# Optimization experiments

Hardware: AMD Instinct MI355X
Metric: run time of the kernel (lower is better)

Reference implementation:

```python
import jax, jax.numpy as jnp
import numpy as np

MAXDISP = 48
NUM_GROUPS = 40
CONCAT_CH = 12
BN_EPS = 1e-5


def conv3d(x, w):
    # x: [B,C,D,H,W], w: [O,I,3,3,3], stride 1, pad 1
    return jax.lax.conv_general_dilated(
        x, w, window_strides=(1, 1, 1), padding=[(1, 1), (1, 1), (1, 1)],
        dimension_numbers=('NCDHW', 'OIDHW', 'NCDHW'))


def bn_relu(x, gamma, beta, mean, var):
    # inference-style BatchNorm3d followed by ReLU
    inv = gamma * jax.lax.rsqrt(var + BN_EPS)
    sh = (1, -1, 1, 1, 1)
    return jax.nn.relu(x * inv.reshape(sh) + (beta - mean * inv).reshape(sh))


def build_volume(lg, rg, lc, rc):
    # Fused gwc + concat volume: for disparity d, valid region is columns [d:].
    # Columns [:d] are zero (matches the torch new_zeros + sliced writes).
    B, Cg, H, W = lg.shape
    cpg = Cg // NUM_GROUPS
    slices = []
    for d in range(MAXDISP):  # fixed structural loop over disparities
        if d == 0:
            l, r, lcc, rcc = lg, rg, lc, rc
        else:
            l = lg[:, :, :, d:]
            r = rg[:, :, :, :W - d]
            lcc = lc[:, :, :, d:]
            rcc = rc[:, :, :, :W - d]
        corr = (l * r).reshape(B, NUM_GROUPS, cpg, H, W - d).mean(axis=2)
        s = jnp.concatenate([corr, lcc, rcc], axis=1)  # [B, G+2Cc, H, W-d]
        if d > 0:
            s = jnp.pad(s, ((0, 0), (0, 0), (0, 0), (d, 0)))
        slices.append(s)
    return jnp.stack(slices, axis=2)  # [B, G+2Cc, D, H, W]


def setup_inputs() -> dict:
    key = jax.random.key(0)
    ks = jax.random.split(key, 10)
    B, H, W = 4, 64, 128
    Cin = NUM_GROUPS + 2 * CONCAT_CH  # 64
    f32 = jnp.float32
    return {
        'left_gwc': jax.random.normal(ks[0], (B, 320, H, W), f32),
        'right_gwc': jax.random.normal(ks[1], (B, 320, H, W), f32),
        'left_concat': jax.random.normal(ks[2], (B, CONCAT_CH, H, W), f32),
        'right_concat': jax.random.normal(ks[3], (B, CONCAT_CH, H, W), f32),
        'w1': jax.random.normal(ks[4], (32, Cin, 3, 3, 3), f32) * 0.05,
        'g1': jnp.ones((32,), f32),
        'b1': jnp.zeros((32,), f32),
        'm1': jnp.zeros((32,), f32),
        'v1': jnp.ones((32,), f32),
        'w2': jax.random.normal(ks[5], (32, 32, 3, 3, 3), f32) * 0.05,
        'g2': jnp.ones((32,), f32),
        'b2': jnp.zeros((32,), f32),
        'm2': jnp.zeros((32,), f32),
        'v2': jnp.ones((32,), f32),
    }


def reference(left_gwc, right_gwc, left_concat, right_concat,
              w1, g1, b1, m1, v1, w2, g2, b2, m2, v2):
    vol = build_volume(left_gwc, right_gwc, left_concat, right_concat)
    x = bn_relu(conv3d(vol, w1), g1, b1, m1, v1)
    x = bn_relu(conv3d(x, w2), g2, b2, m2, v2)
    return x  # [B, 32, D, H, W]
```

## Files before the change

### kernel.cpp

```cpp
#include <hip/hip_runtime.h>
#include <cstdint>
#include <cstddef>

typedef unsigned short u16;
typedef __bf16 bf16x8 __attribute__((ext_vector_type(8)));
typedef float f32x4 __attribute__((ext_vector_type(4)));

#define MAXDISP 48
#define HH 64
#define WW 128

__device__ __forceinline__ float bf2f(unsigned int x) {
    union { unsigned int i; float f; } c; c.i = x << 16; return c.f;
}
__device__ __forceinline__ float bf2f_hi(unsigned int x) {
    union { unsigned int i; float f; } c; c.i = x & 0xffff0000u; return c.f;
}
__device__ __forceinline__ u16 f2bf(float f) {
    union { float f; unsigned int i; } c; c.f = f;
    unsigned int x = c.i;
    return (u16)((x + 0x7fffu + ((x >> 16) & 1u)) >> 16);
}

__global__ __launch_bounds__(256) void wfrag_kernel(
    const float* __restrict__ w, const float* __restrict__ gam,
    const float* __restrict__ bet, const float* __restrict__ mea,
    const float* __restrict__ var,
    u16* __restrict__ dst, float* __restrict__ bias, int CIN, int KC)
{
    int idx = blockIdx.x * 256 + threadIdx.x;
    int n = 9 * 2 * KC * 512;
    if (idx < n) {
        int j    = idx & 7;
        int lane = (idx >> 3) & 63;
        int t2   = idx >> 9;
        int kc   = t2 % KC;
        int t3   = t2 / KC;
        int nt   = t3 & 1;
        int tap  = t3 >> 1;
        int co   = nt * 16 + (lane & 15);
        int qq   = lane >> 4;
        int kw, c;
        if (CIN == 64) { kw = kc >> 1; c = (kc & 1) * 32 + qq * 8 + j; }
        else           { kw = kc;      c = qq * 8 + j; }
        int kd = tap / 3, kh = tap % 3;
        float inv = gam[co] * rsqrtf(var[co] + 1e-5f);
        dst[idx] = f2bf(w[((size_t)co * CIN + c) * 27 + kd * 9 + kh * 3 + kw] * inv);
    }
    if (blockIdx.x == 0 && threadIdx.x < 32) {
        int co = threadIdx.x;
        float inv = gam[co] * rsqrtf(var[co] + 1e-5f);
        bias[co] = bet[co] - mea[co] * inv;
    }
}

#define RS 334
__global__ __launch_bounds__(512) void vol_build_kernel(
    const float* __restrict__ lg, const float* __restrict__ rg,
    const float* __restrict__ lc, const float* __restrict__ rc,
    u16* __restrict__ vol)
{
    __shared__ u16 r_s[128 * RS];
    __shared__ u16 o_s[4 * 128 * 68];

    int bi  = blockIdx.x;
    int h   = bi & 63;
    int dh  = (bi >> 6) & 1;
    int b   = bi >> 7;
    u16* volr = vol + (size_t)(b >> 1) * 50331648;
    int bl  = b & 1;
    int tid = threadIdx.x;
    int w    = tid & 127;
    int part = tid >> 7;

    for (int idx = tid; idx < 320 * 32; idx += 512) {
        int c = idx >> 5, w4 = (idx & 31) << 2;
        const float4 v = *(const float4*)(rg + (((size_t)b * 320 + c) * 64 + h) * 128 + w4);
        r_s[(w4 + 0) * RS + c] = f2bf(v.x);
        r_s[(w4 + 1) * RS + c] = f2bf(v.y);
        r_s[(w4 + 2) * RS + c] = f2bf(v.z);
        r_s[(w4 + 3) * RS + c] = f2bf(v.w);
    }
    for (int idx = tid; idx < 12 * 32; idx += 512) {
        int c = idx >> 5, w4 = (idx & 31) << 2;
        const float4 v = *(const float4*)(rc + (((size_t)b * 12 + c) * 64 + h) * 128 + w4);
        r_s[(w4 + 0) * RS + 320 + c] = f2bf(v.x);
        r_s[(w4 + 1) * RS + 320 + c] = f2bf(v.y);
        r_s[(w4 + 2) * RS + 320 + c] = f2bf(v.z);
        r_s[(w4 + 3) * RS + 320 + c] = f2bf(v.w);
    }
    u16 lcv[12];
    if (part == 0) {
#pragma unroll
        for (int k = 0; k < 12; k++)
            lcv[k] = f2bf(lc[(((size_t)b * 12 + k) * 64 + h) * 128 + w]);
    }
    __syncthreads();

    int d0 = dh * 24;
    for (int dc = 0; dc < 24; dc += 4) {
        for (int gb = 0; gb < 5; gb++) {
            int g0 = part * 10 + gb * 2;
            float lv[2][8];
#pragma unroll
            for (int gg = 0; gg < 2; gg++)
#pragma unroll
                for (int j = 0; j < 8; j++)
                    lv[gg][j] = lg[(((size_t)b * 320 + (g0 + gg) * 8 + j) * 64 + h) * 128 + w];
#pragma unroll
            for (int dl = 0; dl < 4; dl++) {
                int d = d0 + dc + dl;
                union { u16 us[2]; unsigned int u1; } pk;
                pk.us[0] = pk.us[1] = 0;
                if (w >= d) {
#pragma unroll
                    for (int gg = 0; gg < 2; gg++) {
                        float s = 0.f;
                        int base = (w - d) * RS + (g0 + gg) * 8;
#pragma unroll
                        for (int jj = 0; jj < 4; jj++) {
                            unsigned int uu = *(const unsigned int*)&r_s[base + jj * 2];
                            s += lv[gg][jj * 2]     * bf2f(uu & 0xffffu);
                            s += lv[gg][jj * 2 + 1] * bf2f_hi(uu);
                        }
                        pk.us[gg] = f2bf(s * 0.125f);
                    }
                }
                *(unsigned int*)&o_s[(dl * 128 + w) * 68 + g0] = pk.u1;
            }
        }
#pragma unroll
        for (int dl = 0; dl < 4; dl++) {
            int d = d0 + dc + dl;
            union { u16 us[12]; uint2 u2[3]; } z;
            if (part == 0) {
#pragma unroll
                for (int k = 0; k < 12; k++) z.us[k] = (w >= d) ? lcv[k] : (u16)0;
                u16* dst = &o_s[(dl * 128 + w) * 68 + 40];
                *(uint2*)(dst + 0) = z.u2[0];
                *(uint2*)(dst + 4) = z.u2[1];
                *(uint2*)(dst + 8) = z.u2[2];
            } else if (part == 1) {
                if (w >= d) {
                    int base = (w - d) * RS + 320;
#pragma unroll
                    for (int k = 0; k < 12; k++) z.us[k] = r_s[base + k];
                } else {
#pragma unroll
                    for (int k = 0; k < 12; k++) z.us[k] = 0;
                }
                u16* dst = &o_s[(dl * 128 + w) * 68 + 52];
                *(uint2*)(dst + 0) = z.u2[0];
                *(uint2*)(dst + 4) = z.u2[1];
                *(uint2*)(dst + 8) = z.u2[2];
            }
        }
        __syncthreads();
#pragma unroll
        for (int i = 0; i < 8; i++) {
            int idx = i * 512 + tid;
            int dl  = idx >> 10;
            int rem = idx & 1023;
            int ww  = rem >> 3, cg = rem & 7;
            const u16* sp = &o_s[(dl * 128 + ww) * 68 + cg * 8];
            uint2 lo = *(const uint2*)sp;
            uint2 hi = *(const uint2*)(sp + 4);
            uint4 ov = { lo.x, lo.y, hi.x, hi.y };
            int d = d0 + dc + dl;
            *(uint4*)(volr + ((((size_t)bl * 48 + d) * 64 + h) * 128 + ww) * 64
                             + ((cg ^ ((ww + 1) & 7)) << 3)) = ov;
        }
        __syncthreads();
    }
}

__global__ __launch_bounds__(256) void conv1_mfma_kernel(
    const u16* __restrict__ vol, const u16* __restrict__ wf,
    const float* __restrict__ bias, u16* __restrict__ x1)
{
    __shared__ u16 a_s[2][130 * 64];

    int p  = blockIdx.x;
    int bi = (p & 7) * 768 + (p >> 3);
    int h  = bi & 63;
    int t1 = bi >> 6;
    int d  = t1 % 48;
    int bl = t1 / 48;
    int tid  = threadIdx.x;
    int lane = tid & 63, wid = tid >> 6;
    int lm = lane & 15, q = lane >> 4;

    if (tid < 32) {
        uint4 z = { 0, 0, 0, 0 };
        int bb = tid >> 4, t = tid & 15;
        int wp = (t >> 3) ? 129 : 0;
        *(uint4*)&a_s[bb][wp * 64 + (t & 7) * 8] = z;
    }

    f32x4 acc[2][2];
#pragma unroll
    for (int i = 0; i < 2; i++)
#pragma unroll
        for (int j = 0; j < 2; j++) acc[i][j] = { 0.f, 0.f, 0.f, 0.f };

    const size_t blb = (size_t)bl * 48;

    auto stage = [&](int bb, int kd_, int kh_) {
        int dd = d + kd_ - 1; dd = dd < 0 ? 0 : (dd > 47 ? 47 : dd);
        int hh = h + kh_ - 1; hh = hh < 0 ? 0 : (hh > 63 ? 63 : hh);
        const u16* src = vol + ((blb + (size_t)dd) * 64 + hh) * 8192;
        u16* dst = &a_s[bb][64];
#pragma unroll
        for (int i = 0; i < 4; i++) {
            __builtin_amdgcn_global_load_lds(
                (const __attribute__((address_space(1))) unsigned int*)(const void*)(src + (i * 256 + tid) * 8),
                (__attribute__((address_space(3))) unsigned int*)(void*)(dst + (i * 256 + tid) * 8),
                16, 0, 0);
        }
    };

    stage(0, 0, 0);
    __syncthreads();

#pragma unroll
    for (int kd = 0; kd < 3; kd++) {
#pragma unroll
        for (int kh = 0; kh < 3; kh++) {
            const int tap = kd * 3 + kh;
            bool valid = (kd == 0 ? (d > 0) : (kd == 2 ? (d < 47) : true))
                      && (kh == 0 ? (h > 0) : (kh == 2 ? (h < 63) : true));

            bf16x8 bfr[2][6];
            if (valid) {
#pragma unroll
                for (int nt = 0; nt < 2; nt++)
#pragma unroll
                    for (int kc = 0; kc < 6; kc++)
                        bfr[nt][kc] = *(const bf16x8*)(wf + (((size_t)tap * 2 + nt) * 6 + kc) * 512 + lane * 8);
            }
            __builtin_amdgcn_sched_barrier(0);
            if (tap < 8) stage((tap + 1) & 1, (tap + 1) / 3, (tap + 1) % 3);

            if (valid) {
                const u16* as = a_s[tap & 1];
#pragma unroll
                for (int kc = 0; kc < 6; kc++) {
                    int kw = kc >> 1;
                    int cg = (kc & 1) * 4 + q;
#pragma unroll
                    for (int mt = 0; mt < 2; mt++) {
                        int wp = (wid * 2 + mt) * 16 + lm + kw;
                        bf16x8 afr = *(const bf16x8*)&as[wp * 64 + ((cg ^ (wp & 7)) << 3)];
                        acc[mt][0] = __builtin_amdgcn_mfma_f32_16x16x32_bf16(afr, bfr[0][kc], acc[mt][0], 0, 0, 0);
                        acc[mt][1] = __builtin_amdgcn_mfma_f32_16x16x32_bf16(afr, bfr[1][kc], acc[mt][1], 0, 0, 0);
                    }
                }
            }
            __syncthreads();
        }
    }

    u16* xb = x1 + ((blb + d) * 64 + h) * 4096;
#pragma unroll
    for (int mt = 0; mt < 2; mt++)
#pragma unroll
        for (int nt = 0; nt < 2; nt++) {
            int co = nt * 16 + lm;
            float bs = bias[co];
#pragma unroll
            for (int r = 0; r < 4; r++) {
                int w = (wid * 2 + mt) * 16 + q * 4 + r;
                int wp = w + 1, wq = wp >> 1, odd = wp & 1;
                int c16s = (co >> 3) ^ (wq & 3);
                xb[wq * 64 + (odd * 4 + c16s) * 8 + (co & 7) - 32] =
                    f2bf(fmaxf(acc[mt][nt][r] + bs, 0.f));
            }
        }
}

__global__ __launch_bounds__(256) void conv2_mfma_kernel(
    const u16* __restrict__ x1, const u16* __restrict__ wf,
    const float* __restrict__ bias, float* __restrict__ out, int b0)
{
    __shared__ u16 a_s[2][65 * 64];

    int p  = blockIdx.x;
    int bi = (p & 7) * 768 + (p >> 3);
    int h  = bi & 63;
    int t1 = bi >> 6;
    int d  = t1 % 48;
    int bl = t1 / 48;
    int tid  = threadIdx.x;
    int lane = tid & 63, wid = tid >> 6;
    int lm = lane & 15, q = lane >> 4;

    if (tid < 16) {
        uint4 z = { 0, 0, 0, 0 };
        int bb = tid >> 3, t = tid & 7;
        int base = (t >> 2) ? 4128 : 0;
        *(uint4*)&a_s[bb][base + (t & 3) * 8] = z;
    }

    f32x4 acc[2][2];
#pragma unroll
    for (int i = 0; i < 2; i++)
#pragma unroll
        for (int j = 0; j < 2; j++) acc[i][j] = { 0.f, 0.f, 0.f, 0.f };

    const size_t blb = (size_t)bl * 48;

    auto stage = [&](int bb, int kd_, int kh_) {
        int dd = d + kd_ - 1; dd = dd < 0 ? 0 : (dd > 47 ? 47 : dd);
        int hh = h + kh_ - 1; hh = hh < 0 ? 0 : (hh > 63 ? 63 : hh);
        const u16* src = x1 + ((blb + (size_t)dd) * 64 + hh) * 4096;
        u16* dst = &a_s[bb][32];
#pragma unroll
        for (int i = 0; i < 2; i++) {
            __builtin_amdgcn_global_load_lds(
                (const __attribute__((address_space(1))) unsigned int*)(const void*)(src + (i * 256 + tid) * 8),
                (__attribute__((address_space(3))) unsigned int*)(void*)(dst + (i * 256 + tid) * 8),
                16, 0, 0);
        }
    };

    stage(0, 0, 0);
    __syncthreads();

#pragma unroll
    for (int kd = 0; kd < 3; kd++) {
#pragma unroll
        for (int kh = 0; kh < 3; kh++) {
            const int tap = kd * 3 + kh;
            bool valid = (kd == 0 ? (d > 0) : (kd == 2 ? (d < 47) : true))
                      && (kh == 0 ? (h > 0) : (kh == 2 ? (h < 63) : true));

            bf16x8 bfr[2][3];
            if (valid) {
#pragma unroll
                for (int nt = 0; nt < 2; nt++)
#pragma unroll
                    for (int kc = 0; kc < 3; kc++)
                        bfr[nt][kc] = *(const bf16x8*)(wf + (((size_t)tap * 2 + nt) * 3 + kc) * 512 + lane * 8);
            }
            __builtin_amdgcn_sched_barrier(0);
            if (tap < 8) stage((tap + 1) & 1, (tap + 1) / 3, (tap + 1) % 3);

            if (valid) {
                const u16* as = a_s[tap & 1];
#pragma unroll
                for (int kc = 0; kc < 3; kc++) {
                    int kw = kc;
#pragma unroll
                    for (int mt = 0; mt < 2; mt++) {
                        int wp = (wid * 2 + mt) * 16 + lm + kw;
                        int wq = wp >> 1;
                        bf16x8 afr = *(const bf16x8*)&as[wq * 64 + (((wp & 1) * 4 + (q ^ (wq & 3))) << 3)];
                        acc[mt][0] = __builtin_amdgcn_mfma_f32_16x16x32_bf16(afr, bfr[0][kc], acc[mt][0], 0, 0, 0);
                        acc[mt][1] = __builtin_amdgcn_mfma_f32_16x16x32_bf16(afr, bfr[1][kc], acc[mt][1], 0, 0, 0);
                    }
                }
            }
            __syncthreads();
        }
    }

#pragma unroll
    for (int mt = 0; mt < 2; mt++)
#pragma unroll
        for (int nt = 0; nt < 2; nt++) {
            int co = nt * 16 + lm;
            float bs = bias[co];
            float4 o;
            o.x = fmaxf(acc[mt][nt][0] + bs, 0.f);
            o.y = fmaxf(acc[mt][nt][1] + bs, 0.f);
            o.z = fmaxf(acc[mt][nt][2] + bs, 0.f);
            o.w = fmaxf(acc[mt][nt][3] + bs, 0.f);
            int wbase = (wid * 2 + mt) * 16 + q * 4;
            *(float4*)(out + ((((size_t)(b0 + bl) * 32 + co) * 48 + d) * 64 + h) * 128 + wbase) = o;
        }
}

extern "C" void kernel_launch(void* const* d_in, const int* in_sizes, int n_in,
                              void* d_out, int out_size, void* d_ws, size_t ws_size,
                              hipStream_t stream)
{
    const float* lg = (const float*)d_in[0];
    const float* rg = (const float*)d_in[1];
    const float* lc = (const float*)d_in[2];
    const float* rc = (const float*)d_in[3];
    const float* w1 = (const float*)d_in[4];
    const float* g1 = (const float*)d_in[5];
    const float* b1 = (const float*)d_in[6];
    const float* m1 = (const float*)d_in[7];
    const float* v1 = (const float*)d_in[8];
    const float* w2 = (const float*)d_in[9];
    const float* g2 = (const float*)d_in[10];
    const float* b2 = (const float*)d_in[11];
    const float* m2 = (const float*)d_in[12];
    const float* v2 = (const float*)d_in[13];
    (void)in_sizes; (void)n_in; (void)out_size; (void)ws_size;

    char* ws = (char*)d_ws;
    u16*   wf1   = (u16*)ws;
    u16*   wf2   = (u16*)(ws + 110592);
    float* bias1 = (float*)(ws + 165888);
    float* bias2 = (float*)(ws + 166016);
    u16*   x1    = (u16*)(ws + 166144);

    wfrag_kernel<<<216, 256, 0, stream>>>(w1, g1, b1, m1, v1, wf1, bias1, 64, 6);
    wfrag_kernel<<<108, 256, 0, stream>>>(w2, g2, b2, m2, v2, wf2, bias2, 32, 3);

    vol_build_kernel<<<512, 512, 0, stream>>>(lg, rg, lc, rc, (u16*)d_out);
    for (int r = 0; r < 2; r++) {
        u16* vol = (u16*)d_out + (size_t)r * 50331648;
        conv1_mfma_kernel<<<6144, 256, 0, stream>>>(vol, wf1, bias1, x1);
        conv2_mfma_kernel<<<6144, 256, 0, stream>>>(x1, wf2, bias2, (float*)d_out, 2 * r);
    }
}
```

Baseline: 656.7 us.

## Compute four output depths per block to reuse staged input planes

Both conv kernels now assign one output depth per wave and four depths per block, with each wave covering the full width. The block streams six depth planes per kernel row through double-buffered LDS so each staged plane serves several output depths. This halves input staging per output at the cost of waves idling on planes outside their kernel window, larger accumulator register use and fewer blocks.

```diff
diff --git a/kernel.cpp b/kernel.cpp
--- a/kernel.cpp
+++ b/kernel.cpp
@@ -181,11 +181,12 @@
     __shared__ u16 a_s[2][130 * 64];
 
     int p  = blockIdx.x;
-    int bi = (p & 7) * 768 + (p >> 3);
+    int bi = (p & 7) * 192 + (p >> 3);
     int h  = bi & 63;
     int t1 = bi >> 6;
-    int d  = t1 % 48;
-    int bl = t1 / 48;
+    int dt = t1 % 12;
+    int bl = t1 / 12;
+    int d0 = dt * 4;
     int tid  = threadIdx.x;
     int lane = tid & 63, wid = tid >> 6;
     int lm = lane & 15, q = lane >> 4;
@@ -197,17 +198,17 @@
         *(uint4*)&a_s[bb][wp * 64 + (t & 7) * 8] = z;
     }
 
-    f32x4 acc[2][2];
-#pragma unroll
-    for (int i = 0; i < 2; i++)
+    f32x4 acc[8][2];
+#pragma unroll
+    for (int i = 0; i < 8; i++)
 #pragma unroll
         for (int j = 0; j < 2; j++) acc[i][j] = { 0.f, 0.f, 0.f, 0.f };
 
     const size_t blb = (size_t)bl * 48;
 
-    auto stage = [&](int bb, int kd_, int kh_) {
-        int dd = d + kd_ - 1; dd = dd < 0 ? 0 : (dd > 47 ? 47 : dd);
-        int hh = h + kh_ - 1; hh = hh < 0 ? 0 : (hh > 63 ? 63 : hh);
+    auto stage = [&](int bb, int dd, int hh) {
+        dd = dd < 0 ? 0 : (dd > 47 ? 47 : dd);
+        hh = hh < 0 ? 0 : (hh > 63 ? 63 : hh);
         const u16* src = vol + ((blb + (size_t)dd) * 64 + hh) * 8192;
         u16* dst = &a_s[bb][64];
 #pragma unroll
@@ -219,57 +220,62 @@
         }
     };
 
-    stage(0, 0, 0);
+    stage(0, d0 - 1, h - 1);
     __syncthreads();
 
 #pragma unroll
-    for (int kd = 0; kd < 3; kd++) {
-#pragma unroll
-        for (int kh = 0; kh < 3; kh++) {
-            const int tap = kd * 3 + kh;
-            bool valid = (kd == 0 ? (d > 0) : (kd == 2 ? (d < 47) : true))
-                      && (kh == 0 ? (h > 0) : (kh == 2 ? (h < 63) : true));
-
-            bf16x8 bfr[2][6];
-            if (valid) {
-#pragma unroll
-                for (int nt = 0; nt < 2; nt++)
-#pragma unroll
-                    for (int kc = 0; kc < 6; kc++)
-                        bfr[nt][kc] = *(const bf16x8*)(wf + (((size_t)tap * 2 + nt) * 6 + kc) * 512 + lane * 8);
-            }
-            __builtin_amdgcn_sched_barrier(0);
-            if (tap < 8) stage((tap + 1) & 1, (tap + 1) / 3, (tap + 1) % 3);
-
-            if (valid) {
-                const u16* as = a_s[tap & 1];
-#pragma unroll
-                for (int kc = 0; kc < 6; kc++) {
-                    int kw = kc >> 1;
-                    int cg = (kc & 1) * 4 + q;
-#pragma unroll
-                    for (int mt = 0; mt < 2; mt++) {
-                        int wp = (wid * 2 + mt) * 16 + lm + kw;
-                        bf16x8 afr = *(const bf16x8*)&as[wp * 64 + ((cg ^ (wp & 7)) << 3)];
-                        acc[mt][0] = __builtin_amdgcn_mfma_f32_16x16x32_bf16(afr, bfr[0][kc], acc[mt][0], 0, 0, 0);
-                        acc[mt][1] = __builtin_amdgcn_mfma_f32_16x16x32_bf16(afr, bfr[1][kc], acc[mt][1], 0, 0, 0);
-                    }
+    for (int pi = 0; pi < 18; pi++) {
+        const int kh  = pi / 6;
+        const int ddo = pi % 6 - 1;
+        int kd = ddo - wid + 1;
+        bool valid = (kd >= 0) && (kd <= 2)
+                  && (d0 + ddo >= 0) && (d0 + ddo < 48)
+                  && (h + kh - 1 >= 0) && (h + kh - 1 < 64);
+
+        bf16x8 bfr[2][6];
+        if (valid) {
+            int tap = kd * 3 + kh;
+#pragma unroll
+            for (int nt = 0; nt < 2; nt++)
+#pragma unroll
+                for (int kc = 0; kc < 6; kc++)
+                    bfr[nt][kc] = *(const bf16x8*)(wf + (((size_t)tap * 2 + nt) * 6 + kc) * 512 + lane * 8);
+        }
+        __builtin_amdgcn_sched_barrier(0);
+        if (pi < 17) {
+            const int nkh  = (pi + 1) / 6;
+            const int nddo = (pi + 1) % 6 - 1;
+            stage((pi + 1) & 1, d0 + nddo, h + nkh - 1);
+        }
+
+        if (valid) {
+            const u16* as = a_s[pi & 1];
+#pragma unroll
+            for (int kc = 0; kc < 6; kc++) {
+                int kw = kc >> 1;
+                int cg = (kc & 1) * 4 + q;
+#pragma unroll
+                for (int mt = 0; mt < 8; mt++) {
+                    int row = mt * 16 + lm + kw;
+                    bf16x8 afr = *(const bf16x8*)&as[row * 64 + ((cg ^ (row & 7)) << 3)];
+                    acc[mt][0] = __builtin_amdgcn_mfma_f32_16x16x32_bf16(afr, bfr[0][kc], acc[mt][0], 0, 0, 0);
+                    acc[mt][1] = __builtin_amdgcn_mfma_f32_16x16x32_bf16(afr, bfr[1][kc], acc[mt][1], 0, 0, 0);
                 }
             }
-            __syncthreads();
-        }
-    }
-
-    u16* xb = x1 + ((blb + d) * 64 + h) * 4096;
-#pragma unroll
-    for (int mt = 0; mt < 2; mt++)
+        }
+        __syncthreads();
+    }
+
+    u16* xb = x1 + ((blb + d0 + wid) * 64 + h) * 4096;
+#pragma unroll
+    for (int mt = 0; mt < 8; mt++)
 #pragma unroll
         for (int nt = 0; nt < 2; nt++) {
             int co = nt * 16 + lm;
             float bs = bias[co];
 #pragma unroll
             for (int r = 0; r < 4; r++) {
-                int w = (wid * 2 + mt) * 16 + q * 4 + r;
+                int w = mt * 16 + q * 4 + r;
                 int wp = w + 1, wq = wp >> 1, odd = wp & 1;
                 int c16s = (co >> 3) ^ (wq & 3);
                 xb[wq * 64 + (odd * 4 + c16s) * 8 + (co & 7) - 32] =
@@ -285,11 +291,12 @@
     __shared__ u16 a_s[2][65 * 64];
 
     int p  = blockIdx.x;
-    int bi = (p & 7) * 768 + (p >> 3);
+    int bi = (p & 7) * 192 + (p >> 3);
     int h  = bi & 63;
     int t1 = bi >> 6;
-    int d  = t1 % 48;
-    int bl = t1 / 48;
+    int dt = t1 % 12;
+    int bl = t1 / 12;
+    int d0 = dt * 4;
     int tid  = threadIdx.x;
     int lane = tid & 63, wid = tid >> 6;
     int lm = lane & 15, q = lane >> 4;
@@ -301,17 +308,17 @@
         *(uint4*)&a_s[bb][base + (t & 3) * 8] = z;
     }
 
-    f32x4 acc[2][2];
-#pragma unroll
-    for (int i = 0; i < 2; i++)
+    f32x4 acc[8][2];
+#pragma unroll
+    for (int i = 0; i < 8; i++)
 #pragma unroll
         for (int j = 0; j < 2; j++) acc[i][j] = { 0.f, 0.f, 0.f, 0.f };
 
     const size_t blb = (size_t)bl * 48;
 
-    auto stage = [&](int bb, int kd_, int kh_) {
-        int dd = d + kd_ - 1; dd = dd < 0 ? 0 : (dd > 47 ? 47 : dd);
-        int hh = h + kh_ - 1; hh = hh < 0 ? 0 : (hh > 63 ? 63 : hh);
+    auto stage = [&](int bb, int dd, int hh) {
+        dd = dd < 0 ? 0 : (dd > 47 ? 47 : dd);
+        hh = hh < 0 ? 0 : (hh > 63 ? 63 : hh);
         const u16* src = x1 + ((blb + (size_t)dd) * 64 + hh) * 4096;
         u16* dst = &a_s[bb][32];
 #pragma unroll
@@ -323,49 +330,55 @@
         }
     };
 
-    stage(0, 0, 0);
+    stage(0, d0 - 1, h - 1);
     __syncthreads();
 
 #pragma unroll
-    for (int kd = 0; kd < 3; kd++) {
-#pragma unroll
-        for (int kh = 0; kh < 3; kh++) {
-            const int tap = kd * 3 + kh;
-            bool valid = (kd == 0 ? (d > 0) : (kd == 2 ? (d < 47) : true))
-                      && (kh == 0 ? (h > 0) : (kh == 2 ? (h < 63) : true));
-
-            bf16x8 bfr[2][3];
-            if (valid) {
-#pragma unroll
-                for (int nt = 0; nt < 2; nt++)
-#pragma unroll
-                    for (int kc = 0; kc < 3; kc++)
-                        bfr[nt][kc] = *(const bf16x8*)(wf + (((size_t)tap * 2 + nt) * 3 + kc) * 512 + lane * 8);
-            }
-            __builtin_amdgcn_sched_barrier(0);
-            if (tap < 8) stage((tap + 1) & 1, (tap + 1) / 3, (tap + 1) % 3);
-
-            if (valid) {
-                const u16* as = a_s[tap & 1];
-#pragma unroll
-                for (int kc = 0; kc < 3; kc++) {
-                    int kw = kc;
-#pragma unroll
-                    for (int mt = 0; mt < 2; mt++) {
-                        int wp = (wid * 2 + mt) * 16 + lm + kw;
-                        int wq = wp >> 1;
-                        bf16x8 afr = *(const bf16x8*)&as[wq * 64 + (((wp & 1) * 4 + (q ^ (wq & 3))) << 3)];
-                        acc[mt][0] = __builtin_amdgcn_mfma_f32_16x16x32_bf16(afr, bfr[0][kc], acc[mt][0], 0, 0, 0);
-                        acc[mt][1] = __builtin_amdgcn_mfma_f32_16x16x32_bf16(afr, bfr[1][kc], acc[mt][1], 0, 0, 0);
-                    }
+    for (int pi = 0; pi < 18; pi++) {
+        const int kh  = pi / 6;
+        const int ddo = pi % 6 - 1;
+        int kd = ddo - wid + 1;
+        bool valid = (kd >= 0) && (kd <= 2)
+                  && (d0 + ddo >= 0) && (d0 + ddo < 48)
+                  && (h + kh - 1 >= 0) && (h + kh - 1 < 64);
+
+        bf16x8 bfr[2][3];
+        if (valid) {
+            int tap = kd * 3 + kh;
+#pragma unroll
+            for (int nt = 0; nt < 2; nt++)
+#pragma unroll
+                for (int kc = 0; kc < 3; kc++)
+                    bfr[nt][kc] = *(const bf16x8*)(wf + (((size_t)tap * 2 + nt) * 3 + kc) * 512 + lane * 8);
+        }
+        __builtin_amdgcn_sched_barrier(0);
+        if (pi < 17) {
+            const int nkh  = (pi + 1) / 6;
+            const int nddo = (pi + 1) % 6 - 1;
+            stage((pi + 1) & 1, d0 + nddo, h + nkh - 1);
+        }
+
+        if (valid) {
+            const u16* as = a_s[pi & 1];
+#pragma unroll
+            for (int kc = 0; kc < 3; kc++) {
+                int kw = kc;
+#pragma unroll
+                for (int mt = 0; mt < 8; mt++) {
+                    int wp = mt * 16 + lm + kw;
+                    int wq = wp >> 1;
+                    bf16x8 afr = *(const bf16x8*)&as[wq * 64 + (((wp & 1) * 4 + (q ^ (wq & 3))) << 3)];
+                    acc[mt][0] = __builtin_amdgcn_mfma_f32_16x16x32_bf16(afr, bfr[0][kc], acc[mt][0], 0, 0, 0);
+                    acc[mt][1] = __builtin_amdgcn_mfma_f32_16x16x32_bf16(afr, bfr[1][kc], acc[mt][1], 0, 0, 0);
                 }
             }
-            __syncthreads();
-        }
-    }
-
-#pragma unroll
-    for (int mt = 0; mt < 2; mt++)
+        }
+        __syncthreads();
+    }
+
+    int d = d0 + wid;
+#pragma unroll
+    for (int mt = 0; mt < 8; mt++)
 #pragma unroll
         for (int nt = 0; nt < 2; nt++) {
             int co = nt * 16 + lm;
@@ -375,7 +388,7 @@
             o.y = fmaxf(acc[mt][nt][1] + bs, 0.f);
             o.z = fmaxf(acc[mt][nt][2] + bs, 0.f);
             o.w = fmaxf(acc[mt][nt][3] + bs, 0.f);
-            int wbase = (wid * 2 + mt) * 16 + q * 4;
+            int wbase = mt * 16 + q * 4;
             *(float4*)(out + ((((size_t)(b0 + bl) * 32 + co) * 48 + d) * 64 + h) * 128 + wbase) = o;
         }
 }
@@ -413,7 +426,7 @@
     vol_build_kernel<<<512, 512, 0, stream>>>(lg, rg, lc, rc, (u16*)d_out);
     for (int r = 0; r < 2; r++) {
         u16* vol = (u16*)d_out + (size_t)r * 50331648;
-        conv1_mfma_kernel<<<6144, 256, 0, stream>>>(vol, wf1, bias1, x1);
-        conv2_mfma_kernel<<<6144, 256, 0, stream>>>(x1, wf2, bias2, (float*)d_out, 2 * r);
-    }
-}
+        conv1_mfma_kernel<<<1536, 256, 0, stream>>>(vol, wf1, bias1, x1);
+        conv2_mfma_kernel<<<1536, 256, 0, stream>>>(x1, wf2, bias2, (float*)d_out, 2 * r);
+    }
+}
```

Result: slower. 672.4 us (+2.4%).
